# Kernel tuning notes

Hardware: AMD Instinct MI355X
Metric: run time of the kernel (lower is better)

The kernel has to match this reference:

```python
import jax, jax.numpy as jnp
import numpy as np

N_GENES = 8192      # input genes
WM = 4              # width_multiplier: hidden nodes per gene
HID = N_GENES * WM  # 32768 hidden units
N_TF = 1024         # embedding dim (TF activities)
GPT = 64            # target genes per TF in the prior network
BATCH = 256
EPS = 1e-5          # BatchNorm1d eps


def _connectivity():
    # layer1: hidden node h belongs to gene h // WM (fan_in = 1)
    rows1 = np.arange(HID, dtype=np.int32)
    cols1 = (rows1 // WM).astype(np.int32)
    # layer2: fully connected within each gene group (WM x WM blocks)
    rows2 = np.repeat(np.arange(HID, dtype=np.int32), WM)
    cols2 = (((np.arange(HID)[:, None] // WM) * WM) + np.arange(WM)).astype(np.int32).ravel()
    # layer3: each TF connects to all WM nodes of GPT randomly chosen genes
    rng = np.random.default_rng(0)
    genes = rng.integers(0, N_GENES, size=(N_TF, GPT))
    cols3 = (genes[:, :, None] * WM + np.arange(WM)).astype(np.int32).reshape(-1)
    rows3 = np.repeat(np.arange(N_TF, dtype=np.int32), GPT * WM)
    return rows1, cols1, rows2, cols2, rows3, cols3


def _sparse_linear(x, w, b, rows, cols, out_dim):
    # y[b, o] = sum_{e: rows[e]==o} w[e] * x[b, cols[e]] + b[o]
    xe = x[:, cols] * w  # [B, E]
    y = jnp.zeros((x.shape[0], out_dim), x.dtype).at[:, rows].add(xe)
    return y + b


def _batchnorm(x):
    # BatchNorm1d(affine=False), training mode: biased batch var
    m = jnp.mean(x, axis=0)
    v = jnp.var(x, axis=0)
    return (x - m) / jnp.sqrt(v + EPS)


def setup_inputs() -> dict:
    key = jax.random.key(0)
    k = jax.random.split(key, 7)
    rows1, cols1, rows2, cols2, rows3, cols3 = _connectivity()
    inp = {
        "features": jax.random.normal(k[0], (BATCH, N_GENES), jnp.float32),
        "w1": jax.random.normal(k[1], (HID,), jnp.float32),                 # fan_in 1
        "b1": jax.random.normal(k[2], (HID,), jnp.float32) * 0.01,
        "w2": jax.random.normal(k[3], (HID * WM,), jnp.float32) / np.sqrt(WM),
        "b2": jax.random.normal(k[4], (HID,), jnp.float32) * 0.01,
        "w3": jax.random.normal(k[5], (N_TF * GPT * WM,), jnp.float32) / np.sqrt(GPT * WM),
        "b3": jax.random.normal(k[6], (N_TF,), jnp.float32) * 0.01,
        "rows1": jnp.asarray(rows1), "cols1": jnp.asarray(cols1),
        "rows2": jnp.asarray(rows2), "cols2": jnp.asarray(cols2),
        "rows3": jnp.asarray(rows3), "cols3": jnp.asarray(cols3),
    }
    return inp


def reference(features, w1, b1, w2, b2, w3, b3,
              rows1, cols1, rows2, cols2, rows3, cols3):
    h = _sparse_linear(features, w1, b1, rows1, cols1, HID)
    h = _batchnorm(jax.nn.relu(h))
    h = _sparse_linear(h, w2, b2, rows2, cols2, HID)
    h = _batchnorm(jax.nn.relu(h))
    z = _sparse_linear(h, w3, b3, rows3, cols3, N_TF)
    return _batchnorm(z)
```

## Files before the change

kernel.cpp:

```cpp
#include <hip/hip_runtime.h>
#include <cstddef>

#define EPS 1e-5f

constexpr int NG  = 8192;
constexpr int HID = 32768;
constexpr int NTF = 1024;
constexpr int B   = 256;

static __device__ __forceinline__ unsigned short f2bf(float v) {
    union { float f; unsigned u; } a; a.f = v;
    unsigned r = a.u + 0x7fffu + ((a.u >> 16) & 1u);
    return (unsigned short)(r >> 16);
}
static __device__ __forceinline__ float bf2f(unsigned short b) {
    union { unsigned u; float f; } a; a.u = (unsigned)b << 16;
    return a.f;
}

__global__ __launch_bounds__(256) void stats12(
    const float* __restrict__ x,
    const float* __restrict__ w1,
    const float* __restrict__ b1,
    const float* __restrict__ w2,
    const float* __restrict__ b2,
    unsigned short* __restrict__ xTb,
    float* __restrict__ gconst,
    float* __restrict__ inv2g)
{
    const int lane  = threadIdx.x & 63;
    const int slice = threadIdx.x >> 6;
    const int c     = (blockIdx.x << 6) + lane;
    const int g     = c >> 2;
    const int b0    = slice << 6;

    __shared__ float redA[4][64], redB[4][64];
    __shared__ float m1s[64], inv1s[64];
    __shared__ unsigned short xt[16][258];

    const float w1c = w1[c], b1c = b1[c];
    const float* xp = x + (size_t)b0 * NG + g;

    float s = 0.f, s2 = 0.f;
    #pragma unroll 8
    for (int i = 0; i < 64; ++i) {
        float v = xp[(size_t)i * NG];
        unsigned short vb = f2bf(v);
        if ((lane & 3) == 0) xt[lane >> 2][b0 + i] = vb;
        float h = fmaxf(fmaf(w1c, bf2f(vb), b1c), 0.f);
        s += h;
        s2 = fmaf(h, h, s2);
    }
    redA[slice][lane] = s;
    redB[slice][lane] = s2;
    __syncthreads();
    if (slice == 0) {
        float S  = redA[0][lane] + redA[1][lane] + redA[2][lane] + redA[3][lane];
        float S2 = redB[0][lane] + redB[1][lane] + redB[2][lane] + redB[3][lane];
        float m  = S * (1.f / 256.f);
        float v  = fmaf(-m, m, S2 * (1.f / 256.f));
        m1s[lane]   = m;
        inv1s[lane] = rsqrtf(v + EPS);
    }
    __syncthreads();

    const int lbase = lane & ~3;
    const int gbase = g << 2;
    float w1j[4], b1j[4], w2s[4];
    float bconst = b2[c];
    #pragma unroll
    for (int j = 0; j < 4; ++j) {
        w1j[j] = w1[gbase + j];
        b1j[j] = b1[gbase + j];
        float wv = w2[(c << 2) + j] * inv1s[lbase + j];
        w2s[j] = wv;
        bconst = fmaf(-wv, m1s[lbase + j], bconst);
    }

    if (slice == 0) {
        float* rec = gconst + ((size_t)g << 5);
        const int q = c & 3;
        #pragma unroll
        for (int k = 0; k < 4; ++k) rec[8 + (q << 2) + k] = w2s[k];
        rec[24 + q] = bconst;
        if (q == 0) {
            #pragma unroll
            for (int k = 0; k < 4; ++k) { rec[k] = w1j[k]; rec[4 + k] = b1j[k]; }
        }
    }

    #pragma unroll 4
    for (int k = 0; k < 16; ++k)
        xTb[((size_t)blockIdx.x << 12) + (k << 8) + threadIdx.x] = xt[k][threadIdx.x];

    float t2s = 0.f, t2s2 = 0.f;
    const int gl = lane >> 2;
    #pragma unroll 8
    for (int i = 0; i < 64; ++i) {
        float vv = bf2f(xt[gl][b0 + i]);
        float acc = bconst;
        #pragma unroll
        for (int j = 0; j < 4; ++j) {
            float r = fmaxf(fmaf(w1j[j], vv, b1j[j]), 0.f);
            acc = fmaf(w2s[j], r, acc);
        }
        float r2 = fmaxf(acc, 0.f);
        t2s += r2;
        t2s2 = fmaf(r2, r2, t2s2);
    }

    __syncthreads();
    redA[slice][lane] = t2s;
    redB[slice][lane] = t2s2;
    __syncthreads();
    if (slice == 0) {
        float S  = redA[0][lane] + redA[1][lane] + redA[2][lane] + redA[3][lane];
        float S2 = redB[0][lane] + redB[1][lane] + redB[2][lane] + redB[3][lane];
        float m  = S * (1.f / 256.f);
        float v  = fmaf(-m, m, S2 * (1.f / 256.f));
        inv2g[c] = rsqrtf(v + EPS);
    }
}

__global__ __launch_bounds__(256) void tfdot(
    const unsigned short* __restrict__ xTb,
    const float* __restrict__ gconst,
    const float* __restrict__ inv2g,
    const float* __restrict__ w3,
    const int*   __restrict__ cols3,
    float* __restrict__ out)
{
    const int t   = blockIdx.x;
    const int tid = threadIdx.x;

    __shared__ float wls[256];
    __shared__ int   glist[64];
    __shared__ float recs[64][32];
    __shared__ float rs[4], rs2[4];

    {
        const int e   = (t << 8) + tid;
        const int col = cols3[e];
        wls[tid] = w3[e] * inv2g[col];
        if ((tid & 3) == 0) glist[tid >> 2] = col >> 2;
    }
    __syncthreads();

    {
        const int q  = tid & 7;
        const int s0 = tid >> 3;
        const float4* g4 = (const float4*)gconst;
        ((float4*)&recs[s0][0])[q]      = g4[((size_t)glist[s0] << 3) + q];
        ((float4*)&recs[s0 + 32][0])[q] = g4[((size_t)glist[s0 + 32] << 3) + q];
    }
    __syncthreads();

    float z = 0.f;
    #pragma unroll 4
    for (int i = 0; i < 64; ++i) {
        const int g = glist[i];
        float xv = bf2f(xTb[(g << 8) + tid]);

        const float4 w1v = *(const float4*)&recs[i][0];
        const float4 b1v = *(const float4*)&recs[i][4];
        const float4 rC  = *(const float4*)&recs[i][8];
        const float4 rD  = *(const float4*)&recs[i][12];
        const float4 rE  = *(const float4*)&recs[i][16];
        const float4 rF  = *(const float4*)&recs[i][20];
        const float4 bc  = *(const float4*)&recs[i][24];
        const float4 wt  = *(const float4*)&wls[i << 2];

        float h0 = fmaxf(fmaf(w1v.x, xv, b1v.x), 0.f);
        float h1 = fmaxf(fmaf(w1v.y, xv, b1v.y), 0.f);
        float h2 = fmaxf(fmaf(w1v.z, xv, b1v.z), 0.f);
        float h3 = fmaxf(fmaf(w1v.w, xv, b1v.w), 0.f);

        float a0 = bc.x, a1 = bc.y, a2 = bc.z, a3 = bc.w;
        a0 = fmaf(rC.x, h0, a0); a0 = fmaf(rC.y, h1, a0);
        a0 = fmaf(rC.z, h2, a0); a0 = fmaf(rC.w, h3, a0);
        a1 = fmaf(rD.x, h0, a1); a1 = fmaf(rD.y, h1, a1);
        a1 = fmaf(rD.z, h2, a1); a1 = fmaf(rD.w, h3, a1);
        a2 = fmaf(rE.x, h0, a2); a2 = fmaf(rE.y, h1, a2);
        a2 = fmaf(rE.z, h2, a2); a2 = fmaf(rE.w, h3, a2);
        a3 = fmaf(rF.x, h0, a3); a3 = fmaf(rF.y, h1, a3);
        a3 = fmaf(rF.z, h2, a3); a3 = fmaf(rF.w, h3, a3);

        z = fmaf(wt.x, fmaxf(a0, 0.f), z);
        z = fmaf(wt.y, fmaxf(a1, 0.f), z);
        z = fmaf(wt.z, fmaxf(a2, 0.f), z);
        z = fmaf(wt.w, fmaxf(a3, 0.f), z);
    }

    float s = z, s2 = z * z;
    #pragma unroll
    for (int o = 32; o > 0; o >>= 1) {
        s  += __shfl_xor(s, o);
        s2 += __shfl_xor(s2, o);
    }
    if ((tid & 63) == 0) { rs[tid >> 6] = s; rs2[tid >> 6] = s2; }
    __syncthreads();
    float S  = rs[0] + rs[1] + rs[2] + rs[3];
    float S2 = rs2[0] + rs2[1] + rs2[2] + rs2[3];
    float m  = S * (1.f / 256.f);
    float v  = fmaf(-m, m, S2 * (1.f / 256.f));
    out[(size_t)tid * NTF + t] = (z - m) * rsqrtf(v + EPS);
}

extern "C" void kernel_launch(void* const* d_in, const int* in_sizes, int n_in,
                              void* d_out, int out_size, void* d_ws, size_t ws_size,
                              hipStream_t stream) {
    const float* x   = (const float*)d_in[0];
    const float* w1  = (const float*)d_in[1];
    const float* b1  = (const float*)d_in[2];
    const float* w2  = (const float*)d_in[3];
    const float* b2  = (const float*)d_in[4];
    const float* w3  = (const float*)d_in[5];
    const float* b3  = (const float*)d_in[6];  (void)b3;
    const int* cols3 = (const int*)d_in[12];
    float* out = (float*)d_out;

    unsigned short* xTb = (unsigned short*)d_ws;
    float* gconst = (float*)(xTb + (size_t)NG * B);
    float* inv2g  = gconst + (size_t)NG * 32;

    stats12<<<HID / 64, 256, 0, stream>>>(x, w1, b1, w2, b2, xTb, gconst, inv2g);
    tfdot  <<<NTF,      256, 0, stream>>>(xTb, gconst, inv2g, w3, cols3, out);
}
```

Before: 128.9 us.

## Split tfdot gene loop across waves with 4 batch rows per thread

In tfdot, each wave now handles 16 of the 64 genes and each thread processes four consecutive batch rows using a single 8-byte vectorized load of bf16 values. The per-wave partial sums are then combined through a new shared-memory reduction array. The aim is to cut the per-gene LDS record reads by a factor of four for each computed output and to widen the global loads. This adds a shared-memory reduction and an extra barrier, and raises register pressure.

```diff
diff --git a/kernel.cpp b/kernel.cpp
--- a/kernel.cpp
+++ b/kernel.cpp
@@ -132,10 +132,13 @@
 {
     const int t   = blockIdx.x;
     const int tid = threadIdx.x;
+    const int eq  = tid >> 6;
+    const int rq  = tid & 63;
 
     __shared__ float wls[256];
     __shared__ int   glist[64];
     __shared__ float recs[64][32];
+    __shared__ float sred[4][260];
     __shared__ float rs[4], rs2[4];
 
     {
@@ -155,11 +158,15 @@
     }
     __syncthreads();
 
-    float z = 0.f;
+    float z0 = 0.f, z1 = 0.f, z2 = 0.f, z3 = 0.f;
     #pragma unroll 4
-    for (int i = 0; i < 64; ++i) {
+    for (int k = 0; k < 16; ++k) {
+        const int i = (eq << 4) + k;
         const int g = glist[i];
-        float xv = bf2f(xTb[(g << 8) + tid]);
+        uint2 u = *(const uint2*)(xTb + (g << 8) + (rq << 2));
+        union { unsigned v; float f; } p0, p1, p2, p3;
+        p0.v = u.x << 16; p1.v = u.x & 0xffff0000u;
+        p2.v = u.y << 16; p3.v = u.y & 0xffff0000u;
 
         const float4 w1v = *(const float4*)&recs[i][0];
         const float4 b1v = *(const float4*)&recs[i][4];
@@ -170,26 +177,36 @@
         const float4 bc  = *(const float4*)&recs[i][24];
         const float4 wt  = *(const float4*)&wls[i << 2];
 
-        float h0 = fmaxf(fmaf(w1v.x, xv, b1v.x), 0.f);
-        float h1 = fmaxf(fmaf(w1v.y, xv, b1v.y), 0.f);
-        float h2 = fmaxf(fmaf(w1v.z, xv, b1v.z), 0.f);
-        float h3 = fmaxf(fmaf(w1v.w, xv, b1v.w), 0.f);
-
-        float a0 = bc.x, a1 = bc.y, a2 = bc.z, a3 = bc.w;
-        a0 = fmaf(rC.x, h0, a0); a0 = fmaf(rC.y, h1, a0);
-        a0 = fmaf(rC.z, h2, a0); a0 = fmaf(rC.w, h3, a0);
-        a1 = fmaf(rD.x, h0, a1); a1 = fmaf(rD.y, h1, a1);
-        a1 = fmaf(rD.z, h2, a1); a1 = fmaf(rD.w, h3, a1);
-        a2 = fmaf(rE.x, h0, a2); a2 = fmaf(rE.y, h1, a2);
-        a2 = fmaf(rE.z, h2, a2); a2 = fmaf(rE.w, h3, a2);
-        a3 = fmaf(rF.x, h0, a3); a3 = fmaf(rF.y, h1, a3);
-        a3 = fmaf(rF.z, h2, a3); a3 = fmaf(rF.w, h3, a3);
-
-        z = fmaf(wt.x, fmaxf(a0, 0.f), z);
-        z = fmaf(wt.y, fmaxf(a1, 0.f), z);
-        z = fmaf(wt.z, fmaxf(a2, 0.f), z);
-        z = fmaf(wt.w, fmaxf(a3, 0.f), z);
-    }
+        #pragma unroll
+        for (int r = 0; r < 4; ++r) {
+            const float xv = (r == 0) ? p0.f : (r == 1) ? p1.f : (r == 2) ? p2.f : p3.f;
+            float h0 = fmaxf(fmaf(w1v.x, xv, b1v.x), 0.f);
+            float h1 = fmaxf(fmaf(w1v.y, xv, b1v.y), 0.f);
+            float h2 = fmaxf(fmaf(w1v.z, xv, b1v.z), 0.f);
+            float h3 = fmaxf(fmaf(w1v.w, xv, b1v.w), 0.f);
+
+            float a0 = bc.x, a1 = bc.y, a2 = bc.z, a3 = bc.w;
+            a0 = fmaf(rC.x, h0, a0); a0 = fmaf(rC.y, h1, a0);
+            a0 = fmaf(rC.z, h2, a0); a0 = fmaf(rC.w, h3, a0);
+            a1 = fmaf(rD.x, h0, a1); a1 = fmaf(rD.y, h1, a1);
+            a1 = fmaf(rD.z, h2, a1); a1 = fmaf(rD.w, h3, a1);
+            a2 = fmaf(rE.x, h0, a2); a2 = fmaf(rE.y, h1, a2);
+            a2 = fmaf(rE.z, h2, a2); a2 = fmaf(rE.w, h3, a2);
+            a3 = fmaf(rF.x, h0, a3); a3 = fmaf(rF.y, h1, a3);
+            a3 = fmaf(rF.z, h2, a3); a3 = fmaf(rF.w, h3, a3);
+
+            float zi = wt.x * fmaxf(a0, 0.f);
+            zi = fmaf(wt.y, fmaxf(a1, 0.f), zi);
+            zi = fmaf(wt.z, fmaxf(a2, 0.f), zi);
+            zi = fmaf(wt.w, fmaxf(a3, 0.f), zi);
+            if (r == 0) z0 += zi; else if (r == 1) z1 += zi;
+            else if (r == 2) z2 += zi; else z3 += zi;
+        }
+    }
+    *(float4*)&sred[eq][rq << 2] = make_float4(z0, z1, z2, z3);
+    __syncthreads();
+
+    float z = sred[0][tid] + sred[1][tid] + sred[2][tid] + sred[3][tid];
 
     float s = z, s2 = z * z;
     #pragma unroll
```

After: 124.7 us. 1.03x faster.
